# Optimization experiments

Measured on AMD Instinct MI355X. Metric: run time of the kernel, lower is better.

Reference implementation:

```python
import jax, jax.numpy as jnp
import numpy as np

B, S, D, NL, H, KV, F, V, R = 4, 1024, 2048, 2, 16, 4, 8192, 32000, 16
HD = D // H                      # 128, Llama-3 head dim
LORA_SCALE = 32.0 / 16.0         # alpha / r
ROPE_THETA = 500000.0
EPS = 1e-5


def _rope_tables(seq_len, hd):
    inv = 1.0 / (ROPE_THETA ** (jnp.arange(0, hd, 2, dtype=jnp.float32) / hd))
    freqs = jnp.arange(seq_len, dtype=jnp.float32)[:, None] * inv[None, :]   # [S, hd/2]
    emb = jnp.concatenate([freqs, freqs], axis=-1)                           # [S, hd]
    return jnp.cos(emb), jnp.sin(emb)


def _apply_rope(x, cos, sin):
    # x: [B, S, nh, HD]; LLaMA rotate_half convention
    h = x.shape[-1] // 2
    rot = jnp.concatenate([-x[..., h:], x[..., :h]], axis=-1)
    return x * cos[None, :, None, :] + rot * sin[None, :, None, :]


def _rmsnorm(x, w):
    return x * jax.lax.rsqrt(jnp.mean(x * x, axis=-1, keepdims=True) + EPS) * w


def _forward(embed, wq, wk, wv, wo, laq, lbq, lav, lbv, wg, wu, wd, n1, n2, nf,
             input_ids, attention_mask):
    b, s = input_ids.shape
    cos, sin = _rope_tables(s, HD)
    amask = attention_mask.astype(bool)
    # causal AND key-padding mask: [B, 1, S, S]
    mask = jnp.tril(jnp.ones((s, s), bool))[None, None] & amask[:, None, None, :]
    x = embed[input_ids]                                   # [B, S, D]
    for l in range(NL):
        h = _rmsnorm(x, n1[l])
        # base projection + LoRA adapter (q and v only, as in target_modules)
        q = h @ wq[l] + ((h @ laq[l].T) @ lbq[l].T) * LORA_SCALE
        k = h @ wk[l]
        v = h @ wv[l] + ((h @ lav[l].T) @ lbv[l].T) * LORA_SCALE
        q = _apply_rope(q.reshape(b, s, H, HD), cos, sin)
        k = _apply_rope(k.reshape(b, s, KV, HD), cos, sin)
        v = v.reshape(b, s, KV, HD)
        k = jnp.repeat(k, H // KV, axis=2)                 # GQA expand
        v = jnp.repeat(v, H // KV, axis=2)
        scores = jnp.einsum('bqhd,bkhd->bhqk', q, k) / jnp.float32(np.sqrt(HD))
        scores = jnp.where(mask, scores, jnp.float32(-1e9))
        attn = jax.nn.softmax(scores, axis=-1)
        o = jnp.einsum('bhqk,bkhd->bqhd', attn, v).reshape(b, s, D)
        x = x + o @ wo[l]
        h2 = _rmsnorm(x, n2[l])
        x = x + (jax.nn.silu(h2 @ wg[l]) * (h2 @ wu[l])) @ wd[l]
    h = _rmsnorm(x, nf)                                    # final norm -> last_hidden_state
    m = attention_mask.astype(jnp.float32)[..., None]
    return (h * m).sum(axis=1) / jnp.clip(m.sum(axis=1), 1e-9)   # masked mean pool [B, D]


def setup_inputs() -> dict:
    key = jax.random.key(0)
    ks = jax.random.split(key, 14)
    sd = 0.02
    nrm = lambda k, shape: sd * jax.random.normal(k, shape, dtype=jnp.float32)
    return {
        'embed': nrm(ks[0], (V, D)),
        'wq': nrm(ks[1], (NL, D, D)),
        'wk': nrm(ks[2], (NL, D, KV * HD)),
        'wv': nrm(ks[3], (NL, D, KV * HD)),
        'wo': nrm(ks[4], (NL, D, D)),
        'laq': nrm(ks[5], (NL, R, D)),
        'lbq': nrm(ks[6], (NL, D, R)),
        'lav': nrm(ks[7], (NL, R, D)),
        'lbv': nrm(ks[8], (NL, KV * HD, R)),
        'wg': nrm(ks[9], (NL, D, F)),
        'wu': nrm(ks[10], (NL, D, F)),
        'wd': nrm(ks[11], (NL, F, D)),
        'n1': jnp.ones((NL, D), jnp.float32),
        'n2': jnp.ones((NL, D), jnp.float32),
        'nf': jnp.ones((D,), jnp.float32),
        'input_ids': jax.random.randint(ks[12], (B, S), 0, V, dtype=jnp.int32),
        'attention_mask': jnp.ones((B, S), jnp.int32),
    }


def reference(embed, wq, wk, wv, wo, laq, lbq, lav, lbv, wg, wu, wd, n1, n2, nf,
              input_ids, attention_mask):
    return _forward(embed, wq, wk, wv, wo, laq, lbq, lav, lbv, wg, wu, wd,
                    n1, n2, nf, input_ids, attention_mask)
```

## Files before the change

kernel.cpp:

```cpp
#include <hip/hip_runtime.h>
#include <math.h>

#define B_  4
#define S_  1024
#define D_  2048
#define NL_ 2
#define H_  16
#define KV_ 4
#define F_  8192
#define R_  16
#define HD_ 128
#define BS_ (B_*S_)
#define QT2 32
#define KBLK 64
#define NQKV 3072

typedef unsigned short u16;
typedef __attribute__((ext_vector_type(8))) __bf16 bf16x8;
typedef __attribute__((ext_vector_type(4))) float  f32x4;

__device__ __forceinline__ u16 f2bf(float f) {
    unsigned x = __float_as_uint(f);
    unsigned r = (x + 0x7fffu + ((x >> 16) & 1u)) >> 16;
    return (u16)r;
}
__device__ __forceinline__ float bf2f(u16 u) {
    return __uint_as_float(((unsigned)u) << 16);
}

__device__ __forceinline__ void gload16(const void* g, void* l) {
    __builtin_amdgcn_global_load_lds((const __attribute__((address_space(1))) void*)g,
                                     (__attribute__((address_space(3))) void*)l, 16, 0, 0);
}

__global__ void embed_kernel(const float* __restrict__ embed,
                             const int* __restrict__ ids,
                             float* __restrict__ x) {
    int tok = blockIdx.x;
    int id  = ids[tok];
    const float4* src = (const float4*)(embed + (size_t)id * D_);
    float4*       dst = (float4*)(x + (size_t)tok * D_);
    for (int i = threadIdx.x; i < D_/4; i += blockDim.x) dst[i] = src[i];
}

template<int OUTBF>
__global__ __launch_bounds__(256) void rmsnorm_kernel(const float* __restrict__ x,
                                                      const float* __restrict__ w,
                                                      void* __restrict__ out) {
    int row = blockIdx.x;
    const float4* xr = (const float4*)(x + (size_t)row * D_);
    float ss = 0.f;
    for (int i = threadIdx.x; i < D_/4; i += 256) {
        float4 v = xr[i];
        ss += v.x*v.x + v.y*v.y + v.z*v.z + v.w*v.w;
    }
    __shared__ float red[4];
    for (int off = 32; off; off >>= 1) ss += __shfl_down(ss, off);
    if ((threadIdx.x & 63) == 0) red[threadIdx.x >> 6] = ss;
    __syncthreads();
    float tot = red[0] + red[1] + red[2] + red[3];
    float scale = rsqrtf(tot / (float)D_ + 1e-5f);
    const float4* w4 = (const float4*)w;
    for (int i = threadIdx.x; i < D_/4; i += 256) {
        float4 v = xr[i], g = w4[i];
        float a = v.x*scale*g.x, b = v.y*scale*g.y, c = v.z*scale*g.z, d = v.w*scale*g.w;
        if (OUTBF) {
            ushort4 o; o.x = f2bf(a); o.y = f2bf(b); o.z = f2bf(c); o.w = f2bf(d);
            ((ushort4*)((u16*)out + (size_t)row * D_))[i] = o;
        } else {
            float4 o; o.x = a; o.y = b; o.z = c; o.w = d;
            ((float4*)((float*)out + (size_t)row * D_))[i] = o;
        }
    }
}

__global__ __launch_bounds__(256) void convt_kernel(const float* __restrict__ in,
                                                    u16* __restrict__ outT,
                                                    int K, int N) {
    __shared__ float tile[64][65];
    int k0 = blockIdx.y * 64, n0 = blockIdx.x * 64;
    int t = threadIdx.x, r = t >> 4, c4 = (t & 15) * 4;
    #pragma unroll
    for (int p = 0; p < 4; p++) {
        float4 v = *(const float4*)(in + (size_t)(k0 + p * 16 + r) * N + n0 + c4);
        tile[p*16+r][c4]   = v.x; tile[p*16+r][c4+1] = v.y;
        tile[p*16+r][c4+2] = v.z; tile[p*16+r][c4+3] = v.w;
    }
    __syncthreads();
    #pragma unroll
    for (int p = 0; p < 4; p++) {
        int n = p * 16 + r;
        ushort4 o;
        o.x = f2bf(tile[c4][n]);   o.y = f2bf(tile[c4+1][n]);
        o.z = f2bf(tile[c4+2][n]); o.w = f2bf(tile[c4+3][n]);
        *(ushort4*)(outT + (size_t)(n0 + n) * K + k0 + c4) = o;
    }
}

__global__ __launch_bounds__(256) void convt_qkv(const float* __restrict__ wq,
                                                 const float* __restrict__ wk,
                                                 const float* __restrict__ wv,
                                                 const float* __restrict__ wo,
                                                 u16* __restrict__ outT) {
    int z = blockIdx.z;
    int N = (z == 0 || z == 3) ? 2048 : 512;
    if (blockIdx.x * 64 >= N) return;
    const float* in = (z == 0) ? wq : (z == 1 ? wk : (z == 2 ? wv : wo));
    size_t roff = (z == 0) ? 0 : (z == 1 ? 2048 : (z == 2 ? 2560 : 3072));
    u16* out = outT + roff * D_;
    __shared__ float tile[64][65];
    int k0 = blockIdx.y * 64, n0 = blockIdx.x * 64;
    int t = threadIdx.x, r = t >> 4, c4 = (t & 15) * 4;
    #pragma unroll
    for (int p = 0; p < 4; p++) {
        float4 v = *(const float4*)(in + (size_t)(k0 + p * 16 + r) * N + n0 + c4);
        tile[p*16+r][c4]   = v.x; tile[p*16+r][c4+1] = v.y;
        tile[p*16+r][c4+2] = v.z; tile[p*16+r][c4+3] = v.w;
    }
    __syncthreads();
    #pragma unroll
    for (int p = 0; p < 4; p++) {
        int n = p * 16 + r;
        ushort4 o;
        o.x = f2bf(tile[c4][n]);   o.y = f2bf(tile[c4+1][n]);
        o.z = f2bf(tile[c4+2][n]); o.w = f2bf(tile[c4+3][n]);
        *(ushort4*)(out + (size_t)(n0 + n) * D_ + k0 + c4) = o;
    }
}

__global__ __launch_bounds__(256) void convt_gu2(const float* __restrict__ G,
                                                 const float* __restrict__ U,
                                                 u16* __restrict__ outT) {
    __shared__ float tile[64][65];
    int k0 = blockIdx.y * 64, n0 = blockIdx.x * 64;
    int t = threadIdx.x, r = t >> 4, c4 = (t & 15) * 4;
    #pragma unroll
    for (int slot = 0; slot < 2; slot++) {
        const float* in = slot ? U : G;
        if (slot) __syncthreads();
        #pragma unroll
        for (int p = 0; p < 4; p++) {
            float4 v = *(const float4*)(in + (size_t)(k0 + p * 16 + r) * F_ + n0 + c4);
            tile[p*16+r][c4]   = v.x; tile[p*16+r][c4+1] = v.y;
            tile[p*16+r][c4+2] = v.z; tile[p*16+r][c4+3] = v.w;
        }
        __syncthreads();
        #pragma unroll
        for (int p = 0; p < 4; p++) {
            int n = p * 16 + r;
            int orow = n0 + n;
            int wrow = ((orow >> 7) << 8) + slot * 128 + (orow & 127);
            ushort4 o;
            o.x = f2bf(tile[c4][n]);   o.y = f2bf(tile[c4+1][n]);
            o.z = f2bf(tile[c4+2][n]); o.w = f2bf(tile[c4+3][n]);
            *(ushort4*)(outT + (size_t)wrow * D_ + k0 + c4) = o;
        }
    }
}

__global__ __launch_bounds__(256) void gemm_bt_bf16(const u16* __restrict__ A,
                                                    const u16* __restrict__ Bt,
                                                    u16* __restrict__ C,
                                                    int N, int K) {
    __shared__ __align__(16) u16 As[128*64];
    __shared__ __align__(16) u16 Bs[128*64];
    int tid = threadIdx.x, lane = tid & 63;
    int wid = tid >> 6, wm = wid >> 1, wn = wid & 1;
    int m0 = blockIdx.y * 128, n0 = blockIdx.x * 128;
    const u16* Ab = A  + (size_t)m0 * K;
    const u16* Bb = Bt + (size_t)n0 * K;
    f32x4 acc[4][4] = {};
    for (int k0 = 0; k0 < K; k0 += 64) {
        #pragma unroll
        for (int qq = 0; qq < 4; qq++) {
            int u = qq * 256 + tid;
            int row = u >> 3, cu = u & 7, scu = cu ^ (row & 7);
            size_t goff = (size_t)row * K + k0 + scu * 8;
            gload16(Ab + goff, (char*)As + u * 16);
            gload16(Bb + goff, (char*)Bs + u * 16);
        }
        __syncthreads();
        #pragma unroll
        for (int kk = 0; kk < 2; kk++) {
            int cu = kk * 4 + (lane >> 4);
            bf16x8 af[4], bfr[4];
            #pragma unroll
            for (int i = 0; i < 4; i++) {
                int ar = wm * 64 + i * 16 + (lane & 15);
                af[i]  = *(const bf16x8*)((const char*)As + (((ar << 3) | (cu ^ (ar & 7))) << 4));
                int br = wn * 64 + i * 16 + (lane & 15);
                bfr[i] = *(const bf16x8*)((const char*)Bs + (((br << 3) | (cu ^ (br & 7))) << 4));
            }
            #pragma unroll
            for (int i = 0; i < 4; i++)
                #pragma unroll
                for (int j = 0; j < 4; j++)
                    acc[i][j] = __builtin_amdgcn_mfma_f32_16x16x32_bf16(af[i], bfr[j], acc[i][j], 0, 0, 0);
        }
        __syncthreads();
    }
    int r0 = (lane >> 4) * 4, c0 = lane & 15;
    #pragma unroll
    for (int i = 0; i < 4; i++)
        #pragma unroll
        for (int j = 0; j < 4; j++) {
            int row = m0 + wm * 64 + i * 16 + r0;
            int col = n0 + wn * 64 + j * 16 + c0;
            u16* cp = C + (size_t)row * N + col;
            #pragma unroll
            for (int r = 0; r < 4; r++)
                cp[(size_t)r * N] = f2bf(acc[i][j][r]);
        }
}

__global__ __launch_bounds__(512) void gemm_gateup8(const u16* __restrict__ A,
                                                    const u16* __restrict__ Wt,
                                                    u16* __restrict__ act,
                                                    int Nact, int K) {
    __shared__ __align__(16) u16 ring[2][4][8192];
    int tid = threadIdx.x, lane = tid & 63;
    int w = tid >> 6;
    int wm = w >> 2, wn = w & 3;
    int g = lane >> 4, li = lane & 15;
    int m0 = blockIdx.y * 256, n0 = blockIdx.x * 256;
    const u16* Ab = A  + (size_t)m0 * K;
    const u16* Bb = Wt + (size_t)n0 * K;
    int nt = K >> 6;

    f32x4 acc[8][4] = {};

    #define STG(s, t_, kh, P)                                                        \
        do {                                                                         \
            int u_ = (P) * 512 + tid;                                                \
            int j_ = u_ >> 3, cc_ = u_ & 7;                                          \
            int sc_ = cc_ ^ (j_ & 7);                                                \
            int row_ = 2 * j_ + (sc_ >> 2);                                          \
            int kc_ = (t_) * 64 + (kh) * 32 + (sc_ & 3) * 8;                         \
            gload16(Ab + (size_t)row_ * K + kc_, (char*)&ring[0][s][0] + u_ * 16);   \
            gload16(Bb + (size_t)row_ * K + kc_, (char*)&ring[1][s][0] + u_ * 16);   \
        } while (0)

    #define FRAG(op, s, r) (*(const bf16x8*)((const char*)&ring[op][s][0] +          \
        (((((r) >> 1) << 3) | (((((r) & 1) << 2) | g) ^ (((r) >> 1) & 7))) << 4)))

    STG(0, 0, 0, 0); STG(0, 0, 0, 1);
    STG(1, 0, 1, 0); STG(1, 0, 1, 1);
    STG(2, 1, 0, 0); STG(2, 1, 0, 1);

    for (int t = 0; t < nt; t++) {
        int s0  = (2 * t) & 3;
        int s1  = (2 * t + 1) & 3;
        int sW0 = (2 * t + 3) & 3;
        int sW1 = s0;
        bf16x8 afA[4], afB[4], bfr[4];

        if (t == nt - 1) asm volatile("s_waitcnt vmcnt(4)" ::: "memory");
        else             asm volatile("s_waitcnt vmcnt(8)" ::: "memory");
        __builtin_amdgcn_s_barrier();
        __builtin_amdgcn_sched_barrier(0);
        #pragma unroll
        for (int j = 0; j < 4; j++) bfr[j] = FRAG(1, s0, wn * 64 + j * 16 + li);
        #pragma unroll
        for (int i = 0; i < 4; i++) afA[i] = FRAG(0, s0, wm * 128 + i * 16 + li);
        if (t + 1 < nt) STG(sW0, t + 1, 1, 0);
        asm volatile("s_waitcnt lgkmcnt(0)" ::: "memory");
        __builtin_amdgcn_sched_barrier(0);
        __builtin_amdgcn_s_setprio(1);
        #pragma unroll
        for (int i = 0; i < 4; i++)
            #pragma unroll
            for (int j = 0; j < 4; j++)
                acc[i][j] = __builtin_amdgcn_mfma_f32_16x16x32_bf16(afA[i], bfr[j], acc[i][j], 0, 0, 0);
        __builtin_amdgcn_s_setprio(0);
        #pragma unroll
        for (int i = 0; i < 4; i++) afB[i] = FRAG(0, s0, wm * 128 + 64 + i * 16 + li);
        __builtin_amdgcn_sched_barrier(0);

        __builtin_amdgcn_s_barrier();
        __builtin_amdgcn_sched_barrier(0);
        if (t + 1 < nt) STG(sW0, t + 1, 1, 1);
        asm volatile("s_waitcnt lgkmcnt(0)" ::: "memory");
        __builtin_amdgcn_sched_barrier(0);
        __builtin_amdgcn_s_setprio(1);
        #pragma unroll
        for (int i = 0; i < 4; i++)
            #pragma unroll
            for (int j = 0; j < 4; j++)
                acc[4 + i][j] = __builtin_amdgcn_mfma_f32_16x16x32_bf16(afB[i], bfr[j], acc[4 + i][j], 0, 0, 0);
        __builtin_amdgcn_s_setprio(0);

        if (t == nt - 1) asm volatile("s_waitcnt vmcnt(0)" ::: "memory");
        else             asm volatile("s_waitcnt vmcnt(8)" ::: "memory");
        __builtin_amdgcn_s_barrier();
        __builtin_amdgcn_sched_barrier(0);
        #pragma unroll
        for (int j = 0; j < 4; j++) bfr[j] = FRAG(1, s1, wn * 64 + j * 16 + li);
        #pragma unroll
        for (int i = 0; i < 4; i++) afA[i] = FRAG(0, s1, wm * 128 + i * 16 + li);
        if (t + 2 < nt) STG(sW1, t + 2, 0, 0);
        asm volatile("s_waitcnt lgkmcnt(0)" ::: "memory");
        __builtin_amdgcn_sched_barrier(0);
        __builtin_amdgcn_s_setprio(1);
        #pragma unroll
        for (int i = 0; i < 4; i++)
            #pragma unroll
            for (int j = 0; j < 4; j++)
                acc[i][j] = __builtin_amdgcn_mfma_f32_16x16x32_bf16(afA[i], bfr[j], acc[i][j], 0, 0, 0);
        __builtin_amdgcn_s_setprio(0);
        #pragma unroll
        for (int i = 0; i < 4; i++) afB[i] = FRAG(0, s1, wm * 128 + 64 + i * 16 + li);
        __builtin_amdgcn_sched_barrier(0);

        __builtin_amdgcn_s_barrier();
        __builtin_amdgcn_sched_barrier(0);
        if (t + 2 < nt) STG(sW1, t + 2, 0, 1);
        asm volatile("s_waitcnt lgkmcnt(0)" ::: "memory");
        __builtin_amdgcn_sched_barrier(0);
        __builtin_amdgcn_s_setprio(1);
        #pragma unroll
        for (int i = 0; i < 4; i++)
            #pragma unroll
            for (int j = 0; j < 4; j++)
                acc[4 + i][j] = __builtin_amdgcn_mfma_f32_16x16x32_bf16(afB[i], bfr[j], acc[4 + i][j], 0, 0, 0);
        __builtin_amdgcn_s_setprio(0);
    }
    #undef STG
    #undef FRAG

    __syncthreads();
    float* X = (float*)&ring[0][0][0];
    if (wn >= 2) {
        float* Rr = X + (size_t)(wm * 2 + (wn - 2)) * 8192;
        #pragma unroll
        for (int i = 0; i < 8; i++)
            #pragma unroll
            for (int j = 0; j < 4; j++)
                #pragma unroll
                for (int r = 0; r < 4; r++) {
                    int row = i * 16 + g * 4 + r;
                    int col = j * 16 + li;
                    Rr[row * 64 + (col ^ (((row >> 2) & 3) << 4))] = acc[i][j][r];
                }
    }
    __syncthreads();
    if (wn < 2) {
        const float* Rr = X + (size_t)(wm * 2 + wn) * 8192;
        int colbase = (n0 >> 1) + wn * 64;
        #pragma unroll
        for (int i = 0; i < 8; i++)
            #pragma unroll
            for (int j = 0; j < 4; j++)
                #pragma unroll
                for (int r = 0; r < 4; r++) {
                    int row = i * 16 + g * 4 + r;
                    int col = j * 16 + li;
                    float gv = acc[i][j][r];
                    float uv = Rr[row * 64 + (col ^ (((row >> 2) & 3) << 4))];
                    float s = gv / (1.f + __expf(-gv));
                    act[(size_t)(m0 + wm * 128 + row) * Nact + colbase + col] = f2bf(s * uv);
                }
    }
}

__global__ __launch_bounds__(512) void gemm_down_ring(const u16* __restrict__ A,
                                                      const u16* __restrict__ Bt,
                                                      float* __restrict__ C,
                                                      int N, int K) {
    __shared__ __align__(16) u16 ringA[4][8192];
    __shared__ __align__(16) u16 ringB[4][4096];
    int tid = threadIdx.x, lane = tid & 63;
    int w = tid >> 6;
    int wm = w >> 1, wn = w & 1;
    int g = lane >> 4, li = lane & 15;
    int m0 = blockIdx.y * 256, n0 = blockIdx.x * 128;
    const u16* Ab = A  + (size_t)m0 * K;
    const u16* Bb = Bt + (size_t)n0 * K;
    int nt = K >> 6;

    f32x4 acc[4][4] = {};

    #define STGA(s, t_, kh, P)                                                       \
        do {                                                                         \
            int u_ = (P) * 512 + tid;                                                \
            int j_ = u_ >> 3, cc_ = u_ & 7;                                          \
            int sc_ = cc_ ^ (j_ & 7);                                                \
            int row_ = 2 * j_ + (sc_ >> 2);                                          \
            int kc_ = (t_) * 64 + (kh) * 32 + (sc_ & 3) * 8;                         \
            gload16(Ab + (size_t)row_ * K + kc_, (char*)&ringA[s][0] + u_ * 16);     \
        } while (0)
    #define STGB(s, t_, kh)                                                          \
        do {                                                                         \
            int u_ = tid;                                                            \
            int j_ = u_ >> 3, cc_ = u_ & 7;                                          \
            int sc_ = cc_ ^ (j_ & 7);                                                \
            int row_ = 2 * j_ + (sc_ >> 2);                                          \
            int kc_ = (t_) * 64 + (kh) * 32 + (sc_ & 3) * 8;                         \
            gload16(Bb + (size_t)row_ * K + kc_, (char*)&ringB[s][0] + u_ * 16);     \
        } while (0)

    #define FRAGA(s, r) (*(const bf16x8*)((const char*)&ringA[s][0] +                \
        (((((r) >> 1) << 3) | (((((r) & 1) << 2) | g) ^ (((r) >> 1) & 7))) << 4)))
    #define FRAGB(s, r) (*(const bf16x8*)((const char*)&ringB[s][0] +                \
        (((((r) >> 1) << 3) | (((((r) & 1) << 2) | g) ^ (((r) >> 1) & 7))) << 4)))

    STGA(0, 0, 0, 0); STGA(0, 0, 0, 1); STGB(0, 0, 0);
    STGA(1, 0, 1, 0); STGA(1, 0, 1, 1); STGB(1, 0, 1);
    STGA(2, 1, 0, 0); STGA(2, 1, 0, 1); STGB(2, 1, 0);

    for (int t = 0; t < nt; t++) {
        int s0  = (2 * t) & 3;
        int s1  = (2 * t + 1) & 3;
        int sW0 = (2 * t + 3) & 3;
        int sW1 = s0;
        bf16x8 af[4], bfr[4];

        if (t == nt - 1) asm volatile("s_waitcnt vmcnt(3)" ::: "memory");
        else             asm volatile("s_waitcnt vmcnt(6)" ::: "memory");
        __builtin_amdgcn_s_barrier();
        __builtin_amdgcn_sched_barrier(0);
        #pragma unroll
        for (int j = 0; j < 4; j++) bfr[j] = FRAGB(s0, wn * 64 + j * 16 + li);
        #pragma unroll
        for (int i = 0; i < 4; i++) af[i] = FRAGA(s0, wm * 64 + i * 16 + li);
        if (t + 1 < nt) { STGA(sW0, t + 1, 1, 0); STGA(sW0, t + 1, 1, 1); STGB(sW0, t + 1, 1); }
        asm volatile("s_waitcnt lgkmcnt(0)" ::: "memory");
        __builtin_amdgcn_sched_barrier(0);
        __builtin_amdgcn_s_setprio(1);
        #pragma unroll
        for (int i = 0; i < 4; i++)
            #pragma unroll
            for (int j = 0; j < 4; j++)
                acc[i][j] = __builtin_amdgcn_mfma_f32_16x16x32_bf16(af[i], bfr[j], acc[i][j], 0, 0, 0);
        __builtin_amdgcn_s_setprio(0);

        if (t == nt - 1) asm volatile("s_waitcnt vmcnt(0)" ::: "memory");
        else             asm volatile("s_waitcnt vmcnt(6)" ::: "memory");
        __builtin_amdgcn_s_barrier();
        __builtin_amdgcn_sched_barrier(0);
        #pragma unroll
        for (int j = 0; j < 4; j++) bfr[j] = FRAGB(s1, wn * 64 + j * 16 + li);
        #pragma unroll
        for (int i = 0; i < 4; i++) af[i] = FRAGA(s1, wm * 64 + i * 16 + li);
        if (t + 2 < nt) { STGA(sW1, t + 2, 0, 0); STGA(sW1, t + 2, 0, 1); STGB(sW1, t + 2, 0); }
        asm volatile("s_waitcnt lgkmcnt(0)" ::: "memory");
        __builtin_amdgcn_sched_barrier(0);
        __builtin_amdgcn_s_setprio(1);
        #pragma unroll
        for (int i = 0; i < 4; i++)
            #pragma unroll
            for (int j = 0; j < 4; j++)
                acc[i][j] = __builtin_amdgcn_mfma_f32_16x16x32_bf16(af[i], bfr[j], acc[i][j], 0, 0, 0);
        __builtin_amdgcn_s_setprio(0);
    }
    #undef STGA
    #undef STGB
    #undef FRAGA
    #undef FRAGB

    int r0 = g * 4, c0 = li;
    #pragma unroll
    for (int i = 0; i < 4; i++)
        #pragma unroll
        for (int j = 0; j < 4; j++) {
            int row = m0 + wm * 64 + i * 16 + r0;
            int col = n0 + wn * 64 + j * 16 + c0;
            float* cp = C + (size_t)row * N + col;
            #pragma unroll
            for (int r = 0; r < 4; r++)
                cp[(size_t)r * N] += acc[i][j][r];
        }
}

__global__ __launch_bounds__(256) void lora_a2(const u16* __restrict__ h,
                                               const float* __restrict__ laq,
                                               const float* __restrict__ lav,
                                               float* __restrict__ t16q,
                                               float* __restrict__ t16v) {
    const float* la = blockIdx.y ? lav : laq;
    float* t16 = blockIdx.y ? t16v : t16q;
    int r = threadIdx.x >> 4;
    int c = threadIdx.x & 15;
    int row = blockIdx.x * 16 + r;
    const ushort4* hr = (const ushort4*)(h + (size_t)row * D_);
    const float4* lr = (const float4*)(la + (size_t)c * D_);
    float acc = 0.f;
    #pragma unroll 4
    for (int i = 0; i < D_/4; i++) {
        ushort4 a = hr[i]; float4 b = lr[i];
        acc += bf2f(a.x)*b.x + bf2f(a.y)*b.y + bf2f(a.z)*b.z + bf2f(a.w)*b.w;
    }
    t16[(size_t)row * R_ + c] = acc;
}

__global__ void qkconv_rope(const u16* __restrict__ qkvb,
                            const float* __restrict__ t16q,
                            const float* __restrict__ lbq,
                            u16* __restrict__ Qc, u16* __restrict__ Kc) {
    int tok = blockIdx.x, hh = blockIdx.y, t = threadIdx.x;
    int b = tok >> 10, s = tok & (S_ - 1);
    __shared__ float ts[R_];
    if (t < R_) ts[t] = t16q[(size_t)tok * R_ + t];
    __syncthreads();
    float inv = __expf(-(float)t * (13.122363377404328f / 64.0f));
    float f = (float)s * inv;
    float c = __cosf(f), si = __sinf(f);
    float x0, x1;
    u16* dst;
    if (hh < H_) {
        const u16* src = qkvb + (size_t)tok * NQKV + hh * HD_;
        int d0 = hh * HD_ + t;
        float l0 = 0.f, l1 = 0.f;
        const float4* b0 = (const float4*)(lbq + (size_t)d0 * R_);
        const float4* b1 = (const float4*)(lbq + (size_t)(d0 + 64) * R_);
        #pragma unroll
        for (int r4 = 0; r4 < 4; r4++) {
            float4 v0 = b0[r4], v1 = b1[r4];
            l0 += v0.x*ts[r4*4] + v0.y*ts[r4*4+1] + v0.z*ts[r4*4+2] + v0.w*ts[r4*4+3];
            l1 += v1.x*ts[r4*4] + v1.y*ts[r4*4+1] + v1.z*ts[r4*4+2] + v1.w*ts[r4*4+3];
        }
        x0 = bf2f(src[t]) + 2.0f * l0;
        x1 = bf2f(src[t + 64]) + 2.0f * l1;
        dst = Qc + (((size_t)(b * H_ + hh)) * S_ + s) * HD_;
    } else {
        int kh = hh - H_;
        const u16* src = qkvb + (size_t)tok * NQKV + 2048 + kh * HD_;
        x0 = bf2f(src[t]);
        x1 = bf2f(src[t + 64]);
        dst = Kc + (((size_t)(b * KV_ + kh)) * S_ + s) * HD_;
    }
    dst[t]      = f2bf(x0 * c - x1 * si);
    dst[t + 64] = f2bf(x1 * c + x0 * si);
}

__global__ __launch_bounds__(256) void vconv_t(const u16* __restrict__ qkvb,
                                               const float* __restrict__ t16v,
                                               const float* __restrict__ lbv,
                                               u16* __restrict__ Vt) {
    __shared__ float tile[32][33];
    __shared__ float ts[32][16];
    int s0 = blockIdx.x * 32, d0 = blockIdx.y * 32;
    int bk = blockIdx.z;
    int b = bk >> 2, kvh = bk & 3;
    int t = threadIdx.x;
    #pragma unroll
    for (int p = 0; p < 2; p++) {
        int idx = p * 256 + t;
        ts[idx >> 4][idx & 15] = t16v[(size_t)(b * S_ + s0 + (idx >> 4)) * R_ + (idx & 15)];
    }
    int r = t >> 3, c4 = (t & 7) * 4;
    ushort4 v4 = *(const ushort4*)(qkvb + (size_t)(b * S_ + s0 + r) * NQKV + 2560 + kvh * HD_ + d0 + c4);
    __syncthreads();
    float vv[4] = {bf2f(v4.x), bf2f(v4.y), bf2f(v4.z), bf2f(v4.w)};
    #pragma unroll
    for (int e = 0; e < 4; e++) {
        int d = kvh * HD_ + d0 + c4 + e;
        const float4* lr = (const float4*)(lbv + (size_t)d * R_);
        float l = 0.f;
        #pragma unroll
        for (int r4 = 0; r4 < 4; r4++) {
            float4 w = lr[r4];
            l += w.x*ts[r][r4*4] + w.y*ts[r][r4*4+1] + w.z*ts[r][r4*4+2] + w.w*ts[r][r4*4+3];
        }
        vv[e] += 2.0f * l;
    }
    tile[r][c4] = vv[0]; tile[r][c4+1] = vv[1]; tile[r][c4+2] = vv[2]; tile[r][c4+3] = vv[3];
    __syncthreads();
    int dr = t >> 3, s4 = (t & 7) * 4;
    ushort4 o;
    o.x = f2bf(tile[s4][dr]);   o.y = f2bf(tile[s4+1][dr]);
    o.z = f2bf(tile[s4+2][dr]); o.w = f2bf(tile[s4+3][dr]);
    *(ushort4*)(Vt + (((size_t)(b * KV_ + kvh)) * HD_ + d0 + dr) * S_ + s0 + s4) = o;
}

__global__ __launch_bounds__(512) void flash_attn(const u16* __restrict__ Qc,
                                                  const u16* __restrict__ Kc,
                                                  const u16* __restrict__ Vt,
                                                  const int* __restrict__ am,
                                                  u16* __restrict__ o) {
    __shared__ __align__(16) u16 Ks[64 * 128];
    __shared__ __align__(16) u16 Vs[128 * 64];
    __shared__ __align__(16) u16 Ps[8][16][72];
    __shared__ int am_s[KBLK];
    int qt = gridDim.x - 1 - blockIdx.x;
    int kvh = blockIdx.y, b = blockIdx.z;
    int tid = threadIdx.x, lane = tid & 63, w = tid >> 6;
    int g = lane >> 4, li = lane & 15;
    int h = kvh * 4 + (w & 3);
    int qrow0 = qt * QT2 + (w >> 2) * 16;

    bf16x8 qf[4];
    const u16* qb = Qc + (((size_t)(b * H_ + h)) * S_ + qrow0 + li) * HD_;
    #pragma unroll
    for (int dd = 0; dd < 4; dd++) qf[dd] = *(const bf16x8*)(qb + dd * 32 + g * 8);

    float m_r[4], l_r[4];
    f32x4 oacc[8];
    #pragma unroll
    for (int r = 0; r < 4; r++) { m_r[r] = -1e30f; l_r[r] = 0.f; }
    #pragma unroll
    for (int d = 0; d < 8; d++) oacc[d] = (f32x4){0.f, 0.f, 0.f, 0.f};

    const u16* Kg = Kc + ((size_t)(b * KV_ + kvh)) * S_ * HD_;
    const u16* Vg = Vt + ((size_t)(b * KV_ + kvh)) * HD_ * S_;
    int qg0 = qrow0 + g * 4;
    int nkv = (qt * QT2 + QT2 - 1) >> 6;

    for (int kvt = 0; kvt <= nkv; kvt++) {
        int kv0 = kvt * KBLK;
        #pragma unroll
        for (int qq = 0; qq < 2; qq++) {
            int u = qq * 512 + tid;
            int krow = u >> 4, p = u & 15;
            gload16(Kg + (size_t)(kv0 + krow) * HD_ + (p ^ (krow & 7)) * 8, (char*)Ks + u * 16);
            int vrow = u >> 3, pv = u & 7;
            gload16(Vg + (size_t)vrow * S_ + kv0 + (pv ^ (vrow & 7)) * 8, (char*)Vs + u * 16);
        }
        if (tid < KBLK) am_s[tid] = am[b * S_ + kv0 + tid];
        __syncthreads();

        if (kv0 <= qrow0 + 15) {
            float ps[4][4];
            #pragma unroll
            for (int kt = 0; kt < 4; kt++) {
                f32x4 sa = (f32x4){0.f, 0.f, 0.f, 0.f};
                int row = kt * 16 + li;
                #pragma unroll
                for (int dd = 0; dd < 4; dd++) {
                    int c = dd * 4 + g;
                    bf16x8 kf = *(const bf16x8*)((const char*)Ks + ((row * 16 + (c ^ (row & 7))) << 4));
                    sa = __builtin_amdgcn_mfma_f32_16x16x32_bf16(qf[dd], kf, sa, 0, 0, 0);
                }
                int kcol = kv0 + kt * 16 + li;
                int amok = am_s[kt * 16 + li];
                #pragma unroll
                for (int r = 0; r < 4; r++) {
                    float s = sa[r] * 0.08838834764831845f;
                    ps[kt][r] = (amok && kcol <= qg0 + r) ? s : -1e9f;
                }
            }

            float rmax[4], rsum[4], scl[4];
            #pragma unroll
            for (int r = 0; r < 4; r++)
                rmax[r] = fmaxf(fmaxf(ps[0][r], ps[1][r]), fmaxf(ps[2][r], ps[3][r]));
            #pragma unroll
            for (int msk = 1; msk < 16; msk <<= 1)
                #pragma unroll
                for (int r = 0; r < 4; r++) rmax[r] = fmaxf(rmax[r], __shfl_xor(rmax[r], msk));
            #pragma unroll
            for (int r = 0; r < 4; r++) {
                float mn = fmaxf(m_r[r], rmax[r]);
                scl[r] = __expf(m_r[r] - mn);
                m_r[r] = mn;
                rsum[r] = 0.f;
            }
            #pragma unroll
            for (int kt = 0; kt < 4; kt++)
                #pragma unroll
                for (int r = 0; r < 4; r++) {
                    float p = __expf(ps[kt][r] - m_r[r]);
                    ps[kt][r] = p;
                    rsum[r] += p;
                }
            #pragma unroll
            for (int msk = 1; msk < 16; msk <<= 1)
                #pragma unroll
                for (int r = 0; r < 4; r++) rsum[r] += __shfl_xor(rsum[r], msk);
            #pragma unroll
            for (int r = 0; r < 4; r++) l_r[r] = l_r[r] * scl[r] + rsum[r];
            #pragma unroll
            for (int d = 0; d < 8; d++)
                #pragma unroll
                for (int r = 0; r < 4; r++) oacc[d][r] *= scl[r];

            #pragma unroll
            for (int kt = 0; kt < 4; kt++)
                #pragma unroll
                for (int r = 0; r < 4; r++)
                    Ps[w][g * 4 + r][kt * 16 + li] = f2bf(ps[kt][r]);
            bf16x8 pf[2];
            #pragma unroll
            for (int ks = 0; ks < 2; ks++)
                pf[ks] = *(const bf16x8*)&Ps[w][li][ks * 32 + g * 8];

            #pragma unroll
            for (int dblk = 0; dblk < 8; dblk++) {
                int row = dblk * 16 + li;
                #pragma unroll
                for (int ks = 0; ks < 2; ks++) {
                    int c = ks * 4 + g;
                    bf16x8 vf = *(const bf16x8*)((const char*)Vs + ((row * 8 + (c ^ (row & 7))) << 4));
                    oacc[dblk] = __builtin_amdgcn_mfma_f32_16x16x32_bf16(pf[ks], vf, oacc[dblk], 0, 0, 0);
                }
            }
        }
        __syncthreads();
    }

    float invl[4];
    #pragma unroll
    for (int r = 0; r < 4; r++) invl[r] = 1.f / l_r[r];
    #pragma unroll
    for (int dblk = 0; dblk < 8; dblk++)
        #pragma unroll
        for (int r = 0; r < 4; r++) {
            int qrow = qg0 + r;
            o[(((size_t)b * S_ + qrow) * H_ + h) * HD_ + dblk * 16 + li] =
                f2bf(oacc[dblk][r] * invl[r]);
        }
}

__global__ __launch_bounds__(256) void pool_kernel(const float* __restrict__ h,
                                                   const int* __restrict__ am,
                                                   float* __restrict__ out) {
    int b = blockIdx.y;
    int d = blockIdx.x * 256 + threadIdx.x;
    float acc = 0.f, ms = 0.f;
    for (int s = 0; s < S_; s++) {
        float mm = (float)am[b * S_ + s];
        ms  += mm;
        acc += mm * h[((size_t)b * S_ + s) * D_ + d];
    }
    out[(size_t)b * D_ + d] = acc / fmaxf(ms, 1e-9f);
}

extern "C" void kernel_launch(void* const* d_in, const int* in_sizes, int n_in,
                              void* d_out, int out_size, void* d_ws, size_t ws_size,
                              hipStream_t stream) {
    const float* embed = (const float*)d_in[0];
    const float* wq    = (const float*)d_in[1];
    const float* wk    = (const float*)d_in[2];
    const float* wv    = (const float*)d_in[3];
    const float* wo    = (const float*)d_in[4];
    const float* laq   = (const float*)d_in[5];
    const float* lbq   = (const float*)d_in[6];
    const float* lav   = (const float*)d_in[7];
    const float* lbv   = (const float*)d_in[8];
    const float* wg    = (const float*)d_in[9];
    const float* wu    = (const float*)d_in[10];
    const float* wd    = (const float*)d_in[11];
    const float* n1    = (const float*)d_in[12];
    const float* n2    = (const float*)d_in[13];
    const float* nf    = (const float*)d_in[14];
    const int*   ids   = (const int*)d_in[15];
    const int*   am    = (const int*)d_in[16];
    float* out = (float*)d_out;

    char* base = (char*)d_ws;
    float* x    = (float*)base;
    u16*   hbf  = (u16*)(base + 33554432);
    u16*   obf  = (u16*)(base + 50331648);
    char*  Rg   = base + 67108864;
    u16*   qkvb = (u16*)Rg;
    float* t16v = (float*)(base + 117440512);
    u16*   act  = (u16*)Rg;
    float* hf   = (float*)Rg;
    float* t16q = (float*)(base + 134217728);
    u16*   wT0  = (u16*)(base + 134479872);
    u16*   Qc   = (u16*)(base + 201588736);
    u16*   Kc   = (u16*)(base + 218365952);
    u16*   Vtb  = (u16*)(base + 222560256);

    embed_kernel<<<BS_, 256, 0, stream>>>(embed, ids, x);

    for (int l = 0; l < NL_; l++) {
        const float* wql = wq + (size_t)l * D_ * D_;
        const float* wkl = wk + (size_t)l * D_ * (KV_*HD_);
        const float* wvl = wv + (size_t)l * D_ * (KV_*HD_);
        const float* wol = wo + (size_t)l * D_ * D_;
        const float* wgl = wg + (size_t)l * D_ * F_;
        const float* wul = wu + (size_t)l * D_ * F_;
        const float* wdl = wd + (size_t)l * F_ * D_;

        rmsnorm_kernel<1><<<BS_, 256, 0, stream>>>(x, n1 + (size_t)l * D_, hbf);

        convt_qkv<<<dim3(32, 32, 4), 256, 0, stream>>>(wql, wkl, wvl, wol, wT0);
        gemm_bt_bf16<<<dim3(NQKV/128, BS_/128), 256, 0, stream>>>(hbf, wT0, qkvb, NQKV, D_);

        lora_a2<<<dim3(BS_/16, 2), 256, 0, stream>>>(hbf, laq + (size_t)l * R_ * D_,
                                                     lav + (size_t)l * R_ * D_, t16q, t16v);

        qkconv_rope<<<dim3(BS_, H_ + KV_), 64, 0, stream>>>(qkvb, t16q,
                                                            lbq + (size_t)l * D_ * R_, Qc, Kc);
        vconv_t<<<dim3(S_/32, HD_/32, B_*KV_), 256, 0, stream>>>(qkvb, t16v,
                                                                 lbv + (size_t)l * (KV_*HD_) * R_, Vtb);

        flash_attn<<<dim3(S_/QT2, KV_, B_), 512, 0, stream>>>(Qc, Kc, Vtb, am, obf);

        gemm_down_ring<<<dim3(D_/128, BS_/256), 512, 0, stream>>>(obf, wT0 + (size_t)3072 * D_, x, D_, D_);

        rmsnorm_kernel<1><<<BS_, 256, 0, stream>>>(x, n2 + (size_t)l * D_, hbf);
        convt_gu2<<<dim3(F_/64, D_/64), 256, 0, stream>>>(wgl, wul, wT0);
        gemm_gateup8<<<dim3((2*F_)/256, BS_/256), 512, 0, stream>>>(hbf, wT0, act, F_, D_);
        convt_kernel<<<dim3(D_/64, F_/64), 256, 0, stream>>>(wdl, wT0, F_, D_);
        gemm_down_ring<<<dim3(D_/128, BS_/256), 512, 0, stream>>>(act, wT0, x, D_, F_);
    }

    rmsnorm_kernel<0><<<BS_, 256, 0, stream>>>(x, nf, hf);
    pool_kernel<<<dim3(D_/256, B_), 256, 0, stream>>>(hf, am, out);
}
```

Baseline: 1.873 ms.

## Fuse gate/up weight conversion into flash attention launch as extra blocks

The separate gate/up weight transpose-and-convert kernel is merged into the attention launch: blocks numbered 512 and up do the conversion while the first 512 do attention. The attention grid fills only a fraction of the GPU, so the bandwidth-bound conversion can run alongside it. The QKV/O transposed weights move to their own scratch region so they do not clash with the gate/up buffer now being written during attention. The RoPE conversion kernel is also regrouped to handle four heads per 256-thread block, which cuts the block count. The risk is contention for memory bandwidth and shared memory between the two block types.

Measured after the change: 1.934 ms. +3.3%, slower.

```diff
diff --git a/kernel.cpp b/kernel.cpp
--- a/kernel.cpp
+++ b/kernel.cpp
@@ -125,36 +125,6 @@
         o.x = f2bf(tile[c4][n]);   o.y = f2bf(tile[c4+1][n]);
         o.z = f2bf(tile[c4+2][n]); o.w = f2bf(tile[c4+3][n]);
         *(ushort4*)(out + (size_t)(n0 + n) * D_ + k0 + c4) = o;
-    }
-}
-
-__global__ __launch_bounds__(256) void convt_gu2(const float* __restrict__ G,
-                                                 const float* __restrict__ U,
-                                                 u16* __restrict__ outT) {
-    __shared__ float tile[64][65];
-    int k0 = blockIdx.y * 64, n0 = blockIdx.x * 64;
-    int t = threadIdx.x, r = t >> 4, c4 = (t & 15) * 4;
-    #pragma unroll
-    for (int slot = 0; slot < 2; slot++) {
-        const float* in = slot ? U : G;
-        if (slot) __syncthreads();
-        #pragma unroll
-        for (int p = 0; p < 4; p++) {
-            float4 v = *(const float4*)(in + (size_t)(k0 + p * 16 + r) * F_ + n0 + c4);
-            tile[p*16+r][c4]   = v.x; tile[p*16+r][c4+1] = v.y;
-            tile[p*16+r][c4+2] = v.z; tile[p*16+r][c4+3] = v.w;
-        }
-        __syncthreads();
-        #pragma unroll
-        for (int p = 0; p < 4; p++) {
-            int n = p * 16 + r;
-            int orow = n0 + n;
-            int wrow = ((orow >> 7) << 8) + slot * 128 + (orow & 127);
-            ushort4 o;
-            o.x = f2bf(tile[c4][n]);   o.y = f2bf(tile[c4+1][n]);
-            o.z = f2bf(tile[c4+2][n]); o.w = f2bf(tile[c4+3][n]);
-            *(ushort4*)(outT + (size_t)wrow * D_ + k0 + c4) = o;
-        }
     }
 }
 
@@ -492,14 +462,16 @@
     t16[(size_t)row * R_ + c] = acc;
 }
 
-__global__ void qkconv_rope(const u16* __restrict__ qkvb,
-                            const float* __restrict__ t16q,
-                            const float* __restrict__ lbq,
-                            u16* __restrict__ Qc, u16* __restrict__ Kc) {
-    int tok = blockIdx.x, hh = blockIdx.y, t = threadIdx.x;
+__global__ __launch_bounds__(256) void qkconv_rope(const u16* __restrict__ qkvb,
+                                                   const float* __restrict__ t16q,
+                                                   const float* __restrict__ lbq,
+                                                   u16* __restrict__ Qc, u16* __restrict__ Kc) {
+    int tok = blockIdx.x;
+    int hh  = blockIdx.y * 4 + (threadIdx.x >> 6);
+    int t   = threadIdx.x & 63;
     int b = tok >> 10, s = tok & (S_ - 1);
     __shared__ float ts[R_];
-    if (t < R_) ts[t] = t16q[(size_t)tok * R_ + t];
+    if (threadIdx.x < R_) ts[threadIdx.x] = t16q[(size_t)tok * R_ + threadIdx.x];
     __syncthreads();
     float inv = __expf(-(float)t * (13.122363377404328f / 64.0f));
     float f = (float)s * inv;
@@ -572,18 +544,57 @@
     *(ushort4*)(Vt + (((size_t)(b * KV_ + kvh)) * HD_ + d0 + dr) * S_ + s0 + s4) = o;
 }
 
-__global__ __launch_bounds__(512) void flash_attn(const u16* __restrict__ Qc,
+__global__ __launch_bounds__(512) void flash_conv(const u16* __restrict__ Qc,
                                                   const u16* __restrict__ Kc,
                                                   const u16* __restrict__ Vt,
                                                   const int* __restrict__ am,
-                                                  u16* __restrict__ o) {
-    __shared__ __align__(16) u16 Ks[64 * 128];
-    __shared__ __align__(16) u16 Vs[128 * 64];
-    __shared__ __align__(16) u16 Ps[8][16][72];
-    __shared__ int am_s[KBLK];
-    int qt = gridDim.x - 1 - blockIdx.x;
-    int kvh = blockIdx.y, b = blockIdx.z;
-    int tid = threadIdx.x, lane = tid & 63, w = tid >> 6;
+                                                  u16* __restrict__ o,
+                                                  const float* __restrict__ G,
+                                                  const float* __restrict__ U,
+                                                  u16* __restrict__ Wp) {
+    __shared__ __align__(16) char smem[51456];
+    int bid = blockIdx.x;
+    int tid = threadIdx.x;
+
+    if (bid >= 512) {
+        int cid = bid - 512;
+        int n0 = (cid & 127) * 64;
+        int k0 = (cid >> 7) * 64;
+        float (*tile)[65] = (float (*)[65])smem;
+        int r = tid >> 4, c4 = (tid & 15) * 4;
+        #pragma unroll
+        for (int slot = 0; slot < 2; slot++) {
+            const float* in = slot ? U : G;
+            if (slot) __syncthreads();
+            #pragma unroll
+            for (int p = 0; p < 2; p++) {
+                int row = p * 32 + r;
+                float4 v = *(const float4*)(in + (size_t)(k0 + row) * F_ + n0 + c4);
+                tile[row][c4]   = v.x; tile[row][c4+1] = v.y;
+                tile[row][c4+2] = v.z; tile[row][c4+3] = v.w;
+            }
+            __syncthreads();
+            #pragma unroll
+            for (int p = 0; p < 2; p++) {
+                int n = p * 32 + r;
+                int orow = n0 + n;
+                int wrow = ((orow >> 7) << 8) + slot * 128 + (orow & 127);
+                ushort4 ov;
+                ov.x = f2bf(tile[c4][n]);   ov.y = f2bf(tile[c4+1][n]);
+                ov.z = f2bf(tile[c4+2][n]); ov.w = f2bf(tile[c4+3][n]);
+                *(ushort4*)(Wp + (size_t)wrow * D_ + k0 + c4) = ov;
+            }
+        }
+        return;
+    }
+
+    u16* Ks = (u16*)smem;
+    u16* Vs = (u16*)(smem + 16384);
+    u16* Ps = (u16*)(smem + 32768);
+    int* am_s = (int*)(smem + 51200);
+    int qt = 31 - (bid & 31);
+    int kvh = (bid >> 5) & 3, b = bid >> 7;
+    int lane = tid & 63, w = tid >> 6;
     int g = lane >> 4, li = lane & 15;
     int h = kvh * 4 + (w & 3);
     int qrow0 = qt * QT2 + (w >> 2) * 16;
@@ -677,11 +688,11 @@
             for (int kt = 0; kt < 4; kt++)
                 #pragma unroll
                 for (int r = 0; r < 4; r++)
-                    Ps[w][g * 4 + r][kt * 16 + li] = f2bf(ps[kt][r]);
+                    Ps[(size_t)w * 16 * 72 + (g * 4 + r) * 72 + kt * 16 + li] = f2bf(ps[kt][r]);
             bf16x8 pf[2];
             #pragma unroll
             for (int ks = 0; ks < 2; ks++)
-                pf[ks] = *(const bf16x8*)&Ps[w][li][ks * 32 + g * 8];
+                pf[ks] = *(const bf16x8*)&Ps[(size_t)w * 16 * 72 + li * 72 + ks * 32 + g * 8];
 
             #pragma unroll
             for (int dblk = 0; dblk < 8; dblk++) {
@@ -747,19 +758,20 @@
     float* out = (float*)d_out;
 
     char* base = (char*)d_ws;
-    float* x    = (float*)base;
-    u16*   hbf  = (u16*)(base + 33554432);
-    u16*   obf  = (u16*)(base + 50331648);
-    char*  Rg   = base + 67108864;
-    u16*   qkvb = (u16*)Rg;
-    float* t16v = (float*)(base + 117440512);
-    u16*   act  = (u16*)Rg;
-    float* hf   = (float*)Rg;
-    float* t16q = (float*)(base + 134217728);
-    u16*   wT0  = (u16*)(base + 134479872);
-    u16*   Qc   = (u16*)(base + 201588736);
-    u16*   Kc   = (u16*)(base + 218365952);
-    u16*   Vtb  = (u16*)(base + 222560256);
+    float* x     = (float*)base;
+    u16*   hbf   = (u16*)(base + 33554432);
+    u16*   obf   = (u16*)(base + 50331648);
+    char*  Rg    = base + 67108864;
+    u16*   qkvb  = (u16*)Rg;
+    u16*   wQKVO = (u16*)(Rg + 27262976);
+    float* t16v  = (float*)(base + 117440512);
+    u16*   act   = (u16*)Rg;
+    float* hf    = (float*)Rg;
+    float* t16q  = (float*)(base + 134217728);
+    u16*   wT0   = (u16*)(base + 134479872);
+    u16*   Qc    = (u16*)(base + 201588736);
+    u16*   Kc    = (u16*)(base + 218365952);
+    u16*   Vtb   = (u16*)(base + 222560256);
 
     embed_kernel<<<BS_, 256, 0, stream>>>(embed, ids, x);
 
@@ -774,23 +786,23 @@
 
         rmsnorm_kernel<1><<<BS_, 256, 0, stream>>>(x, n1 + (size_t)l * D_, hbf);
 
-        convt_qkv<<<dim3(32, 32, 4), 256, 0, stream>>>(wql, wkl, wvl, wol, wT0);
-        gemm_bt_bf16<<<dim3(NQKV/128, BS_/128), 256, 0, stream>>>(hbf, wT0, qkvb, NQKV, D_);
+        convt_qkv<<<dim3(32, 32, 4), 256, 0, stream>>>(wql, wkl, wvl, wol, wQKVO);
+        gemm_bt_bf16<<<dim3(NQKV/128, BS_/128), 256, 0, stream>>>(hbf, wQKVO, qkvb, NQKV, D_);
 
         lora_a2<<<dim3(BS_/16, 2), 256, 0, stream>>>(hbf, laq + (size_t)l * R_ * D_,
                                                      lav + (size_t)l * R_ * D_, t16q, t16v);
 
-        qkconv_rope<<<dim3(BS_, H_ + KV_), 64, 0, stream>>>(qkvb, t16q,
-                                                            lbq + (size_t)l * D_ * R_, Qc, Kc);
+        qkconv_rope<<<dim3(BS_, 5), 256, 0, stream>>>(qkvb, t16q,
+                                                      lbq + (size_t)l * D_ * R_, Qc, Kc);
         vconv_t<<<dim3(S_/32, HD_/32, B_*KV_), 256, 0, stream>>>(qkvb, t16v,
                                                                  lbv + (size_t)l * (KV_*HD_) * R_, Vtb);
 
-        flash_attn<<<dim3(S_/QT2, KV_, B_), 512, 0, stream>>>(Qc, Kc, Vtb, am, obf);
-
-        gemm_down_ring<<<dim3(D_/128, BS_/256), 512, 0, stream>>>(obf, wT0 + (size_t)3072 * D_, x, D_, D_);
+        flash_conv<<<dim3(512 + 4096), 512, 0, stream>>>(Qc, Kc, Vtb, am, obf,
+                                                         wgl, wul, wT0);
+
+        gemm_down_ring<<<dim3(D_/128, BS_/256), 512, 0, stream>>>(obf, wQKVO + (size_t)3072 * D_, x, D_, D_);
 
         rmsnorm_kernel<1><<<BS_, 256, 0, stream>>>(x, n2 + (size_t)l * D_, hbf);
-        convt_gu2<<<dim3(F_/64, D_/64), 256, 0, stream>>>(wgl, wul, wT0);
         gemm_gateup8<<<dim3((2*F_)/256, BS_/256), 512, 0, stream>>>(hbf, wT0, act, F_, D_);
         convt_kernel<<<dim3(D_/64, F_/64), 256, 0, stream>>>(wdl, wT0, F_, D_);
         gemm_down_ring<<<dim3(D_/128, BS_/256), 512, 0, stream>>>(act, wT0, x, D_, F_);
```
